# Kernel tuning notes

Hardware: AMD Instinct MI355X
Metric: run time of the kernel (lower is better)

The kernel has to match this reference:

```python
import jax, jax.numpy as jnp
import numpy as np

B, S, H, NH, L = 2, 2048, 2048, 16, 512
HD = H // NH  # head_dim = 128


def setup_inputs() -> dict:
    key = jax.random.key(0)
    k1, k2, k3, k4, k5 = jax.random.split(key, 5)
    scale = 0.02  # mimic xavier-scale init
    return {
        "q": jax.random.normal(k1, (B, S, H), dtype=jnp.float32),
        "latent_kv": jax.random.normal(k2, (B, S, L), dtype=jnp.float32),
        "Wq": jax.random.normal(k3, (H, H), dtype=jnp.float32) * scale,
        "Wkv_expand": jax.random.normal(k4, (2 * H, L), dtype=jnp.float32) * scale,
        "Wout": jax.random.normal(k5, (H, H), dtype=jnp.float32) * scale,
    }


def reference(q, latent_kv, Wq, Wkv_expand, Wout):
    b, sq, _ = q.shape
    sk = latent_kv.shape[1]
    # projections (torch Linear: x @ W.T)
    qp = q @ Wq.T                              # [B,Sq,H]
    kv = latent_kv @ Wkv_expand.T              # [B,Sk,2H]
    k, v = jnp.split(kv, 2, axis=-1)           # each [B,Sk,H]
    # split heads -> [B,NH,S,HD]
    qh = qp.reshape(b, sq, NH, HD).transpose(0, 2, 1, 3)
    kh = k.reshape(b, sk, NH, HD).transpose(0, 2, 1, 3)
    vh = v.reshape(b, sk, NH, HD).transpose(0, 2, 1, 3)
    inv_sqrt_d = 1.0 / jnp.sqrt(jnp.float32(HD))
    scores = jnp.einsum("bhqd,bhkd->bhqk", qh, kh) * inv_sqrt_d
    # causal mask (seq_q == seq_k)
    causal = jnp.tril(jnp.ones((sq, sk), dtype=bool))
    scores = jnp.where(causal, scores, jnp.finfo(scores.dtype).min)
    attn = jax.nn.softmax(scores, axis=-1)
    out = jnp.einsum("bhqk,bhkd->bhqd", attn, vh)  # [B,NH,Sq,HD]
    out = out.transpose(0, 2, 1, 3).reshape(b, sq, H)
    return out @ Wout.T
```

## Files before the change

kernel.cpp:

```cpp
#include <hip/hip_runtime.h>

#define SLEN 2048
#define NHEADS 16
#define HDIM 128

typedef __attribute__((ext_vector_type(8))) short bf16x8;
typedef __attribute__((ext_vector_type(4))) float f32x4;
typedef __attribute__((ext_vector_type(16))) float f32x16;

__device__ __forceinline__ unsigned short f2bf(float f) {
  union { float f; unsigned u; } v; v.f = f;
  unsigned r = v.u + 0x7FFFu + ((v.u >> 16) & 1u);
  return (unsigned short)(r >> 16);
}

__device__ __forceinline__ unsigned pkbf(float a, float b) {
  unsigned r;
  asm("v_cvt_pk_bf16_f32 %0, %1, %2" : "=v"(r) : "v"(a), "v"(b));
  return r;
}

__device__ __forceinline__ void gload16(const void* g, void* l) {
  __builtin_amdgcn_global_load_lds(
      (const __attribute__((address_space(1))) unsigned int*)g,
      (__attribute__((address_space(3))) unsigned int*)l, 16, 0, 0);
}

__global__ __launch_bounds__(256) void cvt_f32_bf16(const float* __restrict__ in,
                                                    unsigned short* __restrict__ out,
                                                    int n8) {
  int i = blockIdx.x * 256 + threadIdx.x;
  if (i >= n8) return;
  const float4* p = reinterpret_cast<const float4*>(in) + (size_t)i * 2;
  float4 a = p[0], b = p[1];
  uint4 o;
  o.x = (unsigned)f2bf(a.x) | ((unsigned)f2bf(a.y) << 16);
  o.y = (unsigned)f2bf(a.z) | ((unsigned)f2bf(a.w) << 16);
  o.z = (unsigned)f2bf(b.x) | ((unsigned)f2bf(b.y) << 16);
  o.w = (unsigned)f2bf(b.z) | ((unsigned)f2bf(b.w) << 16);
  reinterpret_cast<uint4*>(out)[i] = o;
}

template <bool OUT_F32>
__global__ __launch_bounds__(256) void gemm_bt(const unsigned short* __restrict__ A,
                                               const unsigned short* __restrict__ B,
                                               void* __restrict__ Cv,
                                               int M, int N, int K) {
  __shared__ unsigned short As[128 * 32];
  __shared__ unsigned short Bs[128 * 32];
  const int tid = threadIdx.x;
  const int lane = tid & 63, wid = tid >> 6;
  const int g = lane >> 4, q = lane & 15;
  const int nbx = N >> 7;
  const int bx = blockIdx.x % nbx, by = blockIdx.x / nbx;
  const int tM = by << 7, tN = bx << 7;
  const int wm = (wid >> 1) * 64, wn = (wid & 1) * 64;

  f32x4 acc[4][4] = {};

  const int o0 = tid * 16;
  const int r0 = o0 >> 6, c0 = (o0 & 63) >> 1;
  const int r1 = r0 + 64;
  const unsigned short* gA0 = A + (size_t)(tM + r0) * K + c0;
  const unsigned short* gA1 = A + (size_t)(tM + r1) * K + c0;
  const unsigned short* gB0 = B + (size_t)(tN + r0) * K + c0;
  const unsigned short* gB1 = B + (size_t)(tN + r1) * K + c0;
  char* lA = (char*)As;
  char* lB = (char*)Bs;
  const int wo = wid * 1024;

  for (int kt = 0; kt < K; kt += 32) {
    gload16(gA0, lA + wo);
    gload16(gA1, lA + 4096 + wo);
    gload16(gB0, lB + wo);
    gload16(gB1, lB + 4096 + wo);
    gA0 += 32; gA1 += 32; gB0 += 32; gB1 += 32;
    __syncthreads();
    bf16x8 af[4], bfr[4];
#pragma unroll
    for (int i = 0; i < 4; ++i)
      af[i] = *(const bf16x8*)&As[(wm + i * 16 + q) * 32 + g * 8];
#pragma unroll
    for (int j = 0; j < 4; ++j)
      bfr[j] = *(const bf16x8*)&Bs[(wn + j * 16 + q) * 32 + g * 8];
#pragma unroll
    for (int i = 0; i < 4; ++i)
#pragma unroll
      for (int j = 0; j < 4; ++j)
        acc[i][j] = __builtin_amdgcn_mfma_f32_16x16x32_bf16(af[i], bfr[j], acc[i][j], 0, 0, 0);
    __syncthreads();
  }

  if constexpr (OUT_F32) {
    float* C = (float*)Cv;
#pragma unroll
    for (int i = 0; i < 4; ++i)
#pragma unroll
      for (int j = 0; j < 4; ++j)
#pragma unroll
        for (int r = 0; r < 4; ++r)
          C[(size_t)(tM + wm + i * 16 + g * 4 + r) * N + (tN + wn + j * 16 + q)] =
              acc[i][j][r];
  } else {
    unsigned short* C = (unsigned short*)Cv;
#pragma unroll
    for (int i = 0; i < 4; ++i)
#pragma unroll
      for (int j = 0; j < 4; ++j)
#pragma unroll
        for (int r = 0; r < 4; ++r)
          C[(size_t)(tM + wm + i * 16 + g * 4 + r) * N + (tN + wn + j * 16 + q)] =
              f2bf(acc[i][j][r]);
  }
}

__global__ __launch_bounds__(256, 2) void mla_attn(const unsigned short* __restrict__ Q,
                                                   const unsigned short* __restrict__ K,
                                                   const unsigned short* __restrict__ VT,
                                                   unsigned short* __restrict__ AO) {
  __shared__ unsigned short Ks[2][64 * 128];
  __shared__ unsigned short Vs[2][128 * 64];

  const int tid = threadIdx.x, lane = tid & 63, w = tid >> 6;
  const int q5 = lane & 31, half = lane >> 5, q7 = lane & 7;
  const int pi = blockIdx.x >> 5, bh = blockIdx.x & 31;
  const int head = bh & 15, b = bh >> 4;
  const int qt = 15 - pi;
  const int nt = 2 * qt + 2;
  const int myq = qt * 128 + w * 32 + q5;

  const unsigned short* Kbase = K + (size_t)(b * 2048) * 2048 + head * 128;
  const unsigned short* Vbase = VT + (size_t)(b * 2048 + head * 128) * 2048;
  const unsigned short* Qrow = Q + (size_t)(b * 2048 + myq) * 2048 + head * 128;

  const int r0 = tid >> 4, c0 = tid & 15;
  const unsigned short* kS = Kbase + (size_t)r0 * 2048 + ((c0 ^ (r0 & 7)) << 3);
  const int d0 = tid >> 3, c3 = tid & 7;
  const unsigned short* vS = Vbase + (size_t)d0 * 2048 + ((c3 ^ (d0 & 7)) << 3);

  bf16x8 qf[8];
#pragma unroll
  for (int ks = 0; ks < 8; ++ks)
    qf[ks] = *(const bf16x8*)((const char*)Qrow + ks * 32 + half * 16);

  {
    unsigned short* kd = &Ks[0][0] + tid * 8;
    unsigned short* vd = &Vs[0][0] + tid * 8;
#pragma unroll
    for (int s = 0; s < 4; ++s) {
      gload16(kS + (size_t)s * 16 * 2048, kd + s * 2048);
      gload16(vS + (size_t)s * 32 * 2048, vd + s * 2048);
    }
  }

  float m2 = -1e30f, l = 0.f;
  f32x16 o[4];
#pragma unroll
  for (int i = 0; i < 16; ++i) { o[0][i] = 0.f; o[1][i] = 0.f; o[2][i] = 0.f; o[3][i] = 0.f; }

  const float sc_f = 0.08838834764831845f;
  const int arow0 = q5 * 256;
  const int vrow0 = q5 * 128;

  for (int kt = 0; kt < nt; ++kt) {
    const int cur = kt & 1;
    asm volatile("s_waitcnt vmcnt(0)" ::: "memory");
    __builtin_amdgcn_s_barrier();

    if (kt + 1 < nt) {
      const int kvb2 = (kt + 1) * 64;
      unsigned short* kd = &Ks[cur ^ 1][0] + tid * 8;
      unsigned short* vd = &Vs[cur ^ 1][0] + tid * 8;
      const unsigned short* ks2 = kS + (size_t)kvb2 * 2048;
      const unsigned short* vs2 = vS + kvb2;
#pragma unroll
      for (int s = 0; s < 4; ++s) {
        gload16(ks2 + (size_t)s * 16 * 2048, kd + s * 2048);
        gload16(vs2 + (size_t)s * 32 * 2048, vd + s * 2048);
      }
    }

    f32x16 st[2];
#pragma unroll
    for (int i = 0; i < 16; ++i) { st[0][i] = 0.f; st[1][i] = 0.f; }
    const char* kb = (const char*)&Ks[cur][0];
#pragma unroll
    for (int ks = 0; ks < 8; ++ks) {
      const int cd = ks * 2 + half;
#pragma unroll
      for (int m = 0; m < 2; ++m) {
        bf16x8 kf = *(const bf16x8*)(kb + arow0 + m * 8192 + ((cd ^ q7) << 4));
        st[m] = __builtin_amdgcn_mfma_f32_32x32x16_bf16(kf, qf[ks], st[m], 0, 0, 0);
      }
    }

    float t[32];
    const int kvb = kt * 64;
    const bool needmask = (kvb + 63 > qt * 128 + w * 32);
#pragma unroll
    for (int m = 0; m < 2; ++m)
#pragma unroll
      for (int r = 0; r < 16; ++r) {
        float s = st[m][r] * sc_f;
        if (needmask) {
          const int kvloc = m * 32 + (r & 3) + 8 * (r >> 2) + 4 * half;
          s = (kvb + kvloc <= myq) ? s : -3e38f;
        }
        t[m * 16 + r] = s;
      }
    float mx = t[0];
#pragma unroll
    for (int i = 1; i < 32; ++i) mx = fmaxf(mx, t[i]);
    mx = fmaxf(mx, __shfl_xor(mx, 32));

    if (!__all(mx <= m2 + 8.f)) {
      const float mnew = fmaxf(m2, mx);
      const float rsc = __expf(m2 - mnew);
      m2 = mnew; l *= rsc;
#pragma unroll
      for (int r = 0; r < 16; ++r) {
        const int rowv = (r & 3) + 8 * (r >> 2) + 4 * half;
        const float f = __shfl(rsc, rowv);
        o[0][r] *= f; o[1][r] *= f; o[2][r] *= f; o[3][r] *= f;
      }
    }

    float ts = 0.f;
#pragma unroll
    for (int i = 0; i < 32; ++i) { t[i] = __expf(t[i] - m2); ts += t[i]; }
    ts += __shfl_xor(ts, 32);
    l += ts;

    unsigned wpk[2][4][2];
#pragma unroll
    for (int m = 0; m < 2; ++m)
#pragma unroll
      for (int r4 = 0; r4 < 4; ++r4) {
        wpk[m][r4][0] = pkbf(t[m * 16 + r4 * 4 + 0], t[m * 16 + r4 * 4 + 1]);
        wpk[m][r4][1] = pkbf(t[m * 16 + r4 * 4 + 2], t[m * 16 + r4 * 4 + 3]);
      }

    const char* vb = (const char*)&Vs[cur][0];
#pragma unroll
    for (int ks = 0; ks < 4; ++ks) {
      const int m = ks >> 1, i = ks & 1;
      const unsigned s0 = half ? wpk[m][2 * i][0] : wpk[m][2 * i + 1][0];
      const unsigned s1 = half ? wpk[m][2 * i][1] : wpk[m][2 * i + 1][1];
      const unsigned rv0 = (unsigned)__shfl_xor((int)s0, 32);
      const unsigned rv1 = (unsigned)__shfl_xor((int)s1, 32);
      const unsigned ow0 = half ? wpk[m][2 * i + 1][0] : wpk[m][2 * i][0];
      const unsigned ow1 = half ? wpk[m][2 * i + 1][1] : wpk[m][2 * i][1];
      union { unsigned u[4]; bf16x8 v; } fr;
      fr.u[0] = half ? rv0 : ow0;
      fr.u[1] = half ? rv1 : ow1;
      fr.u[2] = half ? ow0 : rv0;
      fr.u[3] = half ? ow1 : rv1;
      const int cd = ks * 2 + half;
#pragma unroll
      for (int nf = 0; nf < 4; ++nf) {
        bf16x8 vf = *(const bf16x8*)(vb + vrow0 + nf * 4096 + ((cd ^ q7) << 4));
        o[nf] = __builtin_amdgcn_mfma_f32_32x32x16_bf16(fr.v, vf, o[nf], 0, 0, 0);
      }
    }
  }

  const float linv = 1.0f / l;
  unsigned short* aob = AO + (size_t)(b * 2048) * 2048 + head * 128;
#pragma unroll
  for (int r = 0; r < 16; ++r) {
    const int rowv = (r & 3) + 8 * (r >> 2) + 4 * half;
    const float f = __shfl(linv, rowv);
    const size_t qa = (size_t)(qt * 128 + w * 32 + rowv);
#pragma unroll
    for (int nf = 0; nf < 4; ++nf)
      aob[qa * 2048 + nf * 32 + q5] = f2bf(o[nf][r] * f);
  }
}

extern "C" void kernel_launch(void* const* d_in, const int* in_sizes, int n_in,
                              void* d_out, int out_size, void* d_ws, size_t ws_size,
                              hipStream_t stream) {
  const float* q    = (const float*)d_in[0];
  const float* lat  = (const float*)d_in[1];
  const float* Wq   = (const float*)d_in[2];
  const float* Wkv  = (const float*)d_in[3];
  const float* Wout = (const float*)d_in[4];

  char* ws = (char*)d_ws;
  unsigned short* qbf   = (unsigned short*)(ws);
  unsigned short* aobf  = (unsigned short*)(ws);
  unsigned short* Wqbf  = (unsigned short*)(ws + 16777216);
  unsigned short* latbf = (unsigned short*)(ws + 25165824);
  unsigned short* Wkvbf = (unsigned short*)(ws + 29360128);
  unsigned short* Wobf  = (unsigned short*)(ws + 33554432);
  unsigned short* qpbf  = (unsigned short*)(ws + 41943040);
  unsigned short* Kbf   = (unsigned short*)(ws + 58720256);
  unsigned short* VTbf  = (unsigned short*)(ws + 75497472);
  unsigned short* Wvbf  = Wkvbf + (size_t)2048 * 512;

  cvt_f32_bf16<<<4096, 256, 0, stream>>>(q, qbf, 1048576);
  cvt_f32_bf16<<<2048, 256, 0, stream>>>(Wq, Wqbf, 524288);
  cvt_f32_bf16<<<1024, 256, 0, stream>>>(lat, latbf, 262144);
  cvt_f32_bf16<<<1024, 256, 0, stream>>>(Wkv, Wkvbf, 262144);
  cvt_f32_bf16<<<2048, 256, 0, stream>>>(Wout, Wobf, 524288);

  gemm_bt<false><<<512, 256, 0, stream>>>(qbf, Wqbf, qpbf, 4096, 2048, 2048);
  gemm_bt<false><<<512, 256, 0, stream>>>(latbf, Wkvbf, Kbf, 4096, 2048, 512);
  gemm_bt<false><<<256, 256, 0, stream>>>(Wvbf, latbf, VTbf, 2048, 2048, 512);
  gemm_bt<false><<<256, 256, 0, stream>>>(Wvbf, latbf + (size_t)2048 * 512,
                                          VTbf + (size_t)2048 * 2048, 2048, 2048, 512);
  mla_attn<<<512, 256, 0, stream>>>(qpbf, Kbf, VTbf, aobf);
  gemm_bt<true><<<512, 256, 0, stream>>>(aobf, Wobf, (float*)d_out, 4096, 2048, 2048);
}
```

Baseline: 257.3 us.

## Pair causal q-tiles per attention block, fuse conversions, prioritize MFMA waves

The attention kernel now launches half as many blocks, and each block processes two query tiles (qt = 15-pr and qt = pr). This gives every block the same causal workload and avoids a long tail from blocks with uneven work. The five fp32-to-bf16 conversion launches are merged into one kernel that picks its input by block index, which removes launch overhead. s_setprio is raised around the MFMA loops so compute waves get issue priority. The risks are lower occupancy from only 256 blocks and the serialized second tile losing prefetch overlap at the tile boundary.

```diff
diff --git a/kernel.cpp b/kernel.cpp
--- a/kernel.cpp
+++ b/kernel.cpp
@@ -26,11 +26,26 @@
       (__attribute__((address_space(3))) unsigned int*)l, 16, 0, 0);
 }
 
-__global__ __launch_bounds__(256) void cvt_f32_bf16(const float* __restrict__ in,
-                                                    unsigned short* __restrict__ out,
-                                                    int n8) {
-  int i = blockIdx.x * 256 + threadIdx.x;
-  if (i >= n8) return;
+__global__ __launch_bounds__(256) void cvt_all(const float* __restrict__ q,
+                                               const float* __restrict__ Wq,
+                                               const float* __restrict__ lat,
+                                               const float* __restrict__ Wkv,
+                                               const float* __restrict__ Wout,
+                                               unsigned short* __restrict__ qo,
+                                               unsigned short* __restrict__ Wqo,
+                                               unsigned short* __restrict__ lato,
+                                               unsigned short* __restrict__ Wkvo,
+                                               unsigned short* __restrict__ Wouto) {
+  const int blk = blockIdx.x;
+  const float* in;
+  unsigned short* out;
+  int base;
+  if (blk < 4096)      { in = q;    out = qo;    base = 0; }
+  else if (blk < 6144) { in = Wq;   out = Wqo;   base = 4096; }
+  else if (blk < 7168) { in = lat;  out = lato;  base = 6144; }
+  else if (blk < 8192) { in = Wkv;  out = Wkvo;  base = 7168; }
+  else                 { in = Wout; out = Wouto; base = 8192; }
+  const int i = (blk - base) * 256 + threadIdx.x;
   const float4* p = reinterpret_cast<const float4*>(in) + (size_t)i * 2;
   float4 a = p[0], b = p[1];
   uint4 o;
@@ -123,157 +138,166 @@
 
   const int tid = threadIdx.x, lane = tid & 63, w = tid >> 6;
   const int q5 = lane & 31, half = lane >> 5, q7 = lane & 7;
-  const int pi = blockIdx.x >> 5, bh = blockIdx.x & 31;
+  const int pr = blockIdx.x >> 5, bh = blockIdx.x & 31;
   const int head = bh & 15, b = bh >> 4;
-  const int qt = 15 - pi;
-  const int nt = 2 * qt + 2;
-  const int myq = qt * 128 + w * 32 + q5;
 
   const unsigned short* Kbase = K + (size_t)(b * 2048) * 2048 + head * 128;
   const unsigned short* Vbase = VT + (size_t)(b * 2048 + head * 128) * 2048;
-  const unsigned short* Qrow = Q + (size_t)(b * 2048 + myq) * 2048 + head * 128;
 
   const int r0 = tid >> 4, c0 = tid & 15;
   const unsigned short* kS = Kbase + (size_t)r0 * 2048 + ((c0 ^ (r0 & 7)) << 3);
   const int d0 = tid >> 3, c3 = tid & 7;
   const unsigned short* vS = Vbase + (size_t)d0 * 2048 + ((c3 ^ (d0 & 7)) << 3);
 
-  bf16x8 qf[8];
-#pragma unroll
-  for (int ks = 0; ks < 8; ++ks)
-    qf[ks] = *(const bf16x8*)((const char*)Qrow + ks * 32 + half * 16);
-
-  {
-    unsigned short* kd = &Ks[0][0] + tid * 8;
-    unsigned short* vd = &Vs[0][0] + tid * 8;
-#pragma unroll
-    for (int s = 0; s < 4; ++s) {
-      gload16(kS + (size_t)s * 16 * 2048, kd + s * 2048);
-      gload16(vS + (size_t)s * 32 * 2048, vd + s * 2048);
-    }
-  }
-
-  float m2 = -1e30f, l = 0.f;
-  f32x16 o[4];
-#pragma unroll
-  for (int i = 0; i < 16; ++i) { o[0][i] = 0.f; o[1][i] = 0.f; o[2][i] = 0.f; o[3][i] = 0.f; }
-
   const float sc_f = 0.08838834764831845f;
   const int arow0 = q5 * 256;
   const int vrow0 = q5 * 128;
 
-  for (int kt = 0; kt < nt; ++kt) {
-    const int cur = kt & 1;
-    asm volatile("s_waitcnt vmcnt(0)" ::: "memory");
-    __builtin_amdgcn_s_barrier();
-
-    if (kt + 1 < nt) {
-      const int kvb2 = (kt + 1) * 64;
-      unsigned short* kd = &Ks[cur ^ 1][0] + tid * 8;
-      unsigned short* vd = &Vs[cur ^ 1][0] + tid * 8;
-      const unsigned short* ks2 = kS + (size_t)kvb2 * 2048;
-      const unsigned short* vs2 = vS + kvb2;
+  for (int t2 = 0; t2 < 2; ++t2) {
+    const int qt = t2 ? pr : 15 - pr;
+    const int nt = 2 * qt + 2;
+    const int myq = qt * 128 + w * 32 + q5;
+    const unsigned short* Qrow = Q + (size_t)(b * 2048 + myq) * 2048 + head * 128;
+
+    bf16x8 qf[8];
+#pragma unroll
+    for (int ks = 0; ks < 8; ++ks)
+      qf[ks] = *(const bf16x8*)((const char*)Qrow + ks * 32 + half * 16);
+
+    __syncthreads();
+
+    {
+      unsigned short* kd = &Ks[0][0] + tid * 8;
+      unsigned short* vd = &Vs[0][0] + tid * 8;
 #pragma unroll
       for (int s = 0; s < 4; ++s) {
-        gload16(ks2 + (size_t)s * 16 * 2048, kd + s * 2048);
-        gload16(vs2 + (size_t)s * 32 * 2048, vd + s * 2048);
+        gload16(kS + (size_t)s * 16 * 2048, kd + s * 2048);
+        gload16(vS + (size_t)s * 32 * 2048, vd + s * 2048);
       }
     }
 
-    f32x16 st[2];
-#pragma unroll
-    for (int i = 0; i < 16; ++i) { st[0][i] = 0.f; st[1][i] = 0.f; }
-    const char* kb = (const char*)&Ks[cur][0];
-#pragma unroll
-    for (int ks = 0; ks < 8; ++ks) {
-      const int cd = ks * 2 + half;
-#pragma unroll
-      for (int m = 0; m < 2; ++m) {
-        bf16x8 kf = *(const bf16x8*)(kb + arow0 + m * 8192 + ((cd ^ q7) << 4));
-        st[m] = __builtin_amdgcn_mfma_f32_32x32x16_bf16(kf, qf[ks], st[m], 0, 0, 0);
+    float m2 = -1e30f, l = 0.f;
+    f32x16 o[4];
+#pragma unroll
+    for (int i = 0; i < 16; ++i) { o[0][i] = 0.f; o[1][i] = 0.f; o[2][i] = 0.f; o[3][i] = 0.f; }
+
+    for (int kt = 0; kt < nt; ++kt) {
+      const int cur = kt & 1;
+      asm volatile("s_waitcnt vmcnt(0)" ::: "memory");
+      __builtin_amdgcn_s_barrier();
+
+      if (kt + 1 < nt) {
+        const int kvb2 = (kt + 1) * 64;
+        unsigned short* kd = &Ks[cur ^ 1][0] + tid * 8;
+        unsigned short* vd = &Vs[cur ^ 1][0] + tid * 8;
+        const unsigned short* ks2 = kS + (size_t)kvb2 * 2048;
+        const unsigned short* vs2 = vS + kvb2;
+#pragma unroll
+        for (int s = 0; s < 4; ++s) {
+          gload16(ks2 + (size_t)s * 16 * 2048, kd + s * 2048);
+          gload16(vs2 + (size_t)s * 32 * 2048, vd + s * 2048);
+        }
+      }
+
+      f32x16 st[2];
+#pragma unroll
+      for (int i = 0; i < 16; ++i) { st[0][i] = 0.f; st[1][i] = 0.f; }
+      const char* kb = (const char*)&Ks[cur][0];
+      __builtin_amdgcn_s_setprio(1);
+#pragma unroll
+      for (int ks = 0; ks < 8; ++ks) {
+        const int cd = ks * 2 + half;
+#pragma unroll
+        for (int m = 0; m < 2; ++m) {
+          bf16x8 kf = *(const bf16x8*)(kb + arow0 + m * 8192 + ((cd ^ q7) << 4));
+          st[m] = __builtin_amdgcn_mfma_f32_32x32x16_bf16(kf, qf[ks], st[m], 0, 0, 0);
+        }
+      }
+      __builtin_amdgcn_s_setprio(0);
+
+      float t[32];
+      const int kvb = kt * 64;
+      const bool needmask = (kvb + 63 > qt * 128 + w * 32);
+#pragma unroll
+      for (int m = 0; m < 2; ++m)
+#pragma unroll
+        for (int r = 0; r < 16; ++r) {
+          float s = st[m][r] * sc_f;
+          if (needmask) {
+            const int kvloc = m * 32 + (r & 3) + 8 * (r >> 2) + 4 * half;
+            s = (kvb + kvloc <= myq) ? s : -3e38f;
+          }
+          t[m * 16 + r] = s;
+        }
+      float mx = t[0];
+#pragma unroll
+      for (int i = 1; i < 32; ++i) mx = fmaxf(mx, t[i]);
+      mx = fmaxf(mx, __shfl_xor(mx, 32));
+
+      if (!__all(mx <= m2 + 8.f)) {
+        const float mnew = fmaxf(m2, mx);
+        const float rsc = __expf(m2 - mnew);
+        m2 = mnew; l *= rsc;
+#pragma unroll
+        for (int r = 0; r < 16; ++r) {
+          const int rowv = (r & 3) + 8 * (r >> 2) + 4 * half;
+          const float f = __shfl(rsc, rowv);
+          o[0][r] *= f; o[1][r] *= f; o[2][r] *= f; o[3][r] *= f;
+        }
+      }
+
+      float ts = 0.f;
+#pragma unroll
+      for (int i = 0; i < 32; ++i) { t[i] = __expf(t[i] - m2); ts += t[i]; }
+      ts += __shfl_xor(ts, 32);
+      l += ts;
+
+      unsigned wpk[2][4][2];
+#pragma unroll
+      for (int m = 0; m < 2; ++m)
+#pragma unroll
+        for (int r4 = 0; r4 < 4; ++r4) {
+          wpk[m][r4][0] = pkbf(t[m * 16 + r4 * 4 + 0], t[m * 16 + r4 * 4 + 1]);
+          wpk[m][r4][1] = pkbf(t[m * 16 + r4 * 4 + 2], t[m * 16 + r4 * 4 + 3]);
+        }
+
+      const char* vb = (const char*)&Vs[cur][0];
+#pragma unroll
+      for (int ks = 0; ks < 4; ++ks) {
+        const int m = ks >> 1, i = ks & 1;
+        const unsigned s0 = half ? wpk[m][2 * i][0] : wpk[m][2 * i + 1][0];
+        const unsigned s1 = half ? wpk[m][2 * i][1] : wpk[m][2 * i + 1][1];
+        const unsigned rv0 = (unsigned)__shfl_xor((int)s0, 32);
+        const unsigned rv1 = (unsigned)__shfl_xor((int)s1, 32);
+        const unsigned ow0 = half ? wpk[m][2 * i + 1][0] : wpk[m][2 * i][0];
+        const unsigned ow1 = half ? wpk[m][2 * i + 1][1] : wpk[m][2 * i][1];
+        union { unsigned u[4]; bf16x8 v; } fr;
+        fr.u[0] = half ? rv0 : ow0;
+        fr.u[1] = half ? rv1 : ow1;
+        fr.u[2] = half ? ow0 : rv0;
+        fr.u[3] = half ? ow1 : rv1;
+        const int cd = ks * 2 + half;
+        __builtin_amdgcn_s_setprio(1);
+#pragma unroll
+        for (int nf = 0; nf < 4; ++nf) {
+          bf16x8 vf = *(const bf16x8*)(vb + vrow0 + nf * 4096 + ((cd ^ q7) << 4));
+          o[nf] = __builtin_amdgcn_mfma_f32_32x32x16_bf16(fr.v, vf, o[nf], 0, 0, 0);
+        }
+        __builtin_amdgcn_s_setprio(0);
       }
     }
 
-    float t[32];
-    const int kvb = kt * 64;
-    const bool needmask = (kvb + 63 > qt * 128 + w * 32);
-#pragma unroll
-    for (int m = 0; m < 2; ++m)
-#pragma unroll
-      for (int r = 0; r < 16; ++r) {
-        float s = st[m][r] * sc_f;
-        if (needmask) {
-          const int kvloc = m * 32 + (r & 3) + 8 * (r >> 2) + 4 * half;
-          s = (kvb + kvloc <= myq) ? s : -3e38f;
-        }
-        t[m * 16 + r] = s;
-      }
-    float mx = t[0];
-#pragma unroll
-    for (int i = 1; i < 32; ++i) mx = fmaxf(mx, t[i]);
-    mx = fmaxf(mx, __shfl_xor(mx, 32));
-
-    if (!__all(mx <= m2 + 8.f)) {
-      const float mnew = fmaxf(m2, mx);
-      const float rsc = __expf(m2 - mnew);
-      m2 = mnew; l *= rsc;
-#pragma unroll
-      for (int r = 0; r < 16; ++r) {
-        const int rowv = (r & 3) + 8 * (r >> 2) + 4 * half;
-        const float f = __shfl(rsc, rowv);
-        o[0][r] *= f; o[1][r] *= f; o[2][r] *= f; o[3][r] *= f;
-      }
+    const float linv = 1.0f / l;
+    unsigned short* aob = AO + (size_t)(b * 2048) * 2048 + head * 128;
+#pragma unroll
+    for (int r = 0; r < 16; ++r) {
+      const int rowv = (r & 3) + 8 * (r >> 2) + 4 * half;
+      const float f = __shfl(linv, rowv);
+      const size_t qa = (size_t)(qt * 128 + w * 32 + rowv);
+#pragma unroll
+      for (int nf = 0; nf < 4; ++nf)
+        aob[qa * 2048 + nf * 32 + q5] = f2bf(o[nf][r] * f);
     }
-
-    float ts = 0.f;
-#pragma unroll
-    for (int i = 0; i < 32; ++i) { t[i] = __expf(t[i] - m2); ts += t[i]; }
-    ts += __shfl_xor(ts, 32);
-    l += ts;
-
-    unsigned wpk[2][4][2];
-#pragma unroll
-    for (int m = 0; m < 2; ++m)
-#pragma unroll
-      for (int r4 = 0; r4 < 4; ++r4) {
-        wpk[m][r4][0] = pkbf(t[m * 16 + r4 * 4 + 0], t[m * 16 + r4 * 4 + 1]);
-        wpk[m][r4][1] = pkbf(t[m * 16 + r4 * 4 + 2], t[m * 16 + r4 * 4 + 3]);
-      }
-
-    const char* vb = (const char*)&Vs[cur][0];
-#pragma unroll
-    for (int ks = 0; ks < 4; ++ks) {
-      const int m = ks >> 1, i = ks & 1;
-      const unsigned s0 = half ? wpk[m][2 * i][0] : wpk[m][2 * i + 1][0];
-      const unsigned s1 = half ? wpk[m][2 * i][1] : wpk[m][2 * i + 1][1];
-      const unsigned rv0 = (unsigned)__shfl_xor((int)s0, 32);
-      const unsigned rv1 = (unsigned)__shfl_xor((int)s1, 32);
-      const unsigned ow0 = half ? wpk[m][2 * i + 1][0] : wpk[m][2 * i][0];
-      const unsigned ow1 = half ? wpk[m][2 * i + 1][1] : wpk[m][2 * i][1];
-      union { unsigned u[4]; bf16x8 v; } fr;
-      fr.u[0] = half ? rv0 : ow0;
-      fr.u[1] = half ? rv1 : ow1;
-      fr.u[2] = half ? ow0 : rv0;
-      fr.u[3] = half ? ow1 : rv1;
-      const int cd = ks * 2 + half;
-#pragma unroll
-      for (int nf = 0; nf < 4; ++nf) {
-        bf16x8 vf = *(const bf16x8*)(vb + vrow0 + nf * 4096 + ((cd ^ q7) << 4));
-        o[nf] = __builtin_amdgcn_mfma_f32_32x32x16_bf16(fr.v, vf, o[nf], 0, 0, 0);
-      }
-    }
-  }
-
-  const float linv = 1.0f / l;
-  unsigned short* aob = AO + (size_t)(b * 2048) * 2048 + head * 128;
-#pragma unroll
-  for (int r = 0; r < 16; ++r) {
-    const int rowv = (r & 3) + 8 * (r >> 2) + 4 * half;
-    const float f = __shfl(linv, rowv);
-    const size_t qa = (size_t)(qt * 128 + w * 32 + rowv);
-#pragma unroll
-    for (int nf = 0; nf < 4; ++nf)
-      aob[qa * 2048 + nf * 32 + q5] = f2bf(o[nf][r] * f);
   }
 }
 
@@ -298,17 +322,14 @@
   unsigned short* VTbf  = (unsigned short*)(ws + 75497472);
   unsigned short* Wvbf  = Wkvbf + (size_t)2048 * 512;
 
-  cvt_f32_bf16<<<4096, 256, 0, stream>>>(q, qbf, 1048576);
-  cvt_f32_bf16<<<2048, 256, 0, stream>>>(Wq, Wqbf, 524288);
-  cvt_f32_bf16<<<1024, 256, 0, stream>>>(lat, latbf, 262144);
-  cvt_f32_bf16<<<1024, 256, 0, stream>>>(Wkv, Wkvbf, 262144);
-  cvt_f32_bf16<<<2048, 256, 0, stream>>>(Wout, Wobf, 524288);
+  cvt_all<<<10240, 256, 0, stream>>>(q, Wq, lat, Wkv, Wout,
+                                     qbf, Wqbf, latbf, Wkvbf, Wobf);
 
   gemm_bt<false><<<512, 256, 0, stream>>>(qbf, Wqbf, qpbf, 4096, 2048, 2048);
   gemm_bt<false><<<512, 256, 0, stream>>>(latbf, Wkvbf, Kbf, 4096, 2048, 512);
   gemm_bt<false><<<256, 256, 0, stream>>>(Wvbf, latbf, VTbf, 2048, 2048, 512);
   gemm_bt<false><<<256, 256, 0, stream>>>(Wvbf, latbf + (size_t)2048 * 512,
                                           VTbf + (size_t)2048 * 2048, 2048, 2048, 512);
-  mla_attn<<<512, 256, 0, stream>>>(qpbf, Kbf, VTbf, aobf);
+  mla_attn<<<256, 256, 0, stream>>>(qpbf, Kbf, VTbf, aobf);
   gemm_bt<true><<<512, 256, 0, stream>>>(aobf, Wobf, (float*)d_out, 4096, 2048, 2048);
 }
```

Result: slower. 263.6 us (+2.5%).
